# Kernel optimization log

Measured on AMD Instinct MI355X. Metric: run time of the kernel, lower is better.

## Reference

```python
import jax, jax.numpy as jnp
import numpy as np

LAMBDA_S = 1.0   # options['lambda_s']
NITER = 100      # options['iter_ihs']

_HS_FILTER = jnp.array([[1/12, 1/6, 1/12],
                        [1/6,  0.0, 1/6 ],
                        [1/12, 1/6, 1/12]], dtype=jnp.float32)


def _smooth(f):
    # f: [n, h, w] -> 3x3 Horn-Schunck weighted average, zero padding (== torch conv2d padding=1)
    k = _HS_FILTER.reshape(1, 1, 3, 3)  # [out_c, in_c, kh, kw]
    return jax.lax.conv_general_dilated(f[:, None], k, window_strides=(1, 1), padding='SAME')[:, 0]


def setup_inputs() -> dict:
    key = jax.random.key(0)
    k1, k2 = jax.random.split(key)
    n, h, w = 8, 256, 256
    x = jax.random.normal(k1, (n, 3, h, w), dtype=jnp.float32)            # [I_t, I_x, I_y]
    old_estimate = jax.random.normal(k2, (n, 2, h, w), dtype=jnp.float32)  # warm-start (u, v)
    return {"x": x, "old_estimate": old_estimate}


def reference(x, old_estimate):
    # x: [n,3,h,w]; old_estimate: [n,2,h,w]
    I_t, I_x, I_y = x[:, 0], x[:, 1], x[:, 2]
    denom = LAMBDA_S ** 2 + I_x ** 2 + I_y ** 2  # iteration-invariant
    u0, v0 = old_estimate[:, 0], old_estimate[:, 1]  # warm_ihs=True

    def step(carry, _):
        u, v = carry
        u_bar = _smooth(u)
        v_bar = _smooth(v)
        der = (I_x * u_bar + I_y * v_bar + I_t) / denom
        return (u_bar - I_x * der, v_bar - I_y * der), None

    (u, v), _ = jax.lax.scan(step, (u0, v0), None, length=NITER)
    return jnp.stack((u, v), axis=1)  # [n,2,h,w]
```

## Files before the change

### kernel.cpp

```cpp
#include <hip/hip_runtime.h>

typedef unsigned long long ull;

#define HH 256
#define WW 256
#define PLANE (HH*WW)
#define TILE_R 32
#define TILE_C 64
#define TT 8
#define ER (TILE_R + 2*TT)
#define EC (TILE_C + 2*TT)
#define NCP (EC/2)
#define NRG 12
#define RPT (ER/NRG)
#define NTHR 512
#define LSZ (4 + ER*EC*2 + 4)

#define RING_OFS (2u*1024u*1024u)
#define FLAG_OFS (4u*1024u*1024u)
#define RIMG (HH*(WW/2)*4)

__global__ __launch_bounds__(NTHR, 2)
void hs_mega(const float* __restrict__ x,
             const float* __restrict__ est,
             float* __restrict__ out,
             float* __restrict__ ws)
{
    __shared__ __align__(16) float s0[LSZ];
    __shared__ __align__(16) float s1[LSZ];

    const int img = blockIdx.x, cs = blockIdx.y, rb = blockIdx.z;
    const int tid = threadIdx.x;
    const int er0 = rb*TILE_R - TT;
    const int ec0 = cs*TILE_C - TT;
    const int blin = (img*4 + cs)*8 + rb;
    unsigned* flags = (unsigned*)(ws + FLAG_OFS);

    int nb = -1;
    if (tid < 8) {
        int t = (tid < 4) ? tid : tid + 1;
        int dr = t/3 - 1, dc = t%3 - 1;
        int nrb = rb + dr, ncs = cs + dc;
        if (nrb >= 0 && nrb < 8 && ncs >= 0 && ncs < 4)
            nb = (img*4 + ncs)*8 + nrb;
    }

    const int cp = tid % NCP;
    const int rg = tid / NCP;
    const bool active = (rg < NRG);
    const int r0   = (active ? rg : 0) * RPT;
    const int fb   = 4 + 4*cp;

    float2 ca[RPT], cb[RPT], cc[RPT], cd[RPT], ce[RPT];
    {
        const float* __restrict__ xit = x + img*3*PLANE;
        const float* __restrict__ xix = xit + PLANE;
        const float* __restrict__ xiy = xix + PLANE;
        #pragma unroll
        for (int i = 0; i < RPT; ++i) {
            int gr = er0 + r0 + i;
            #pragma unroll
            for (int j = 0; j < 2; ++j) {
                int gc = ec0 + 2*cp + j;
                float A=0.f, B=0.f, C=0.f, D=0.f, E=0.f;
                if (active && gr >= 0 && gr < HH && gc >= 0 && gc < WW) {
                    int q = gr*WW + gc;
                    float it = xit[q], ix = xix[q], iy = xiy[q];
                    float rd = 1.0f / (1.0f + ix*ix + iy*iy);
                    const float s12 = 1.0f/12.0f;
                    A = (1.0f - ix*ix*rd) * s12;
                    B = (ix*iy*rd) * s12;
                    C = ix*it*rd;
                    D = (1.0f - iy*iy*rd) * s12;
                    E = iy*it*rd;
                }
                if (j == 0) { ca[i].x=A; cb[i].x=B; cc[i].x=C; cd[i].x=D; ce[i].x=E; }
                else        { ca[i].y=A; cb[i].y=B; cc[i].y=C; cd[i].y=D; ce[i].y=E; }
            }
        }
    }

    {
        const float* __restrict__ eu = est + img*2*PLANE;
        const float* __restrict__ ev = eu + PLANE;
        for (int k = tid; k < ER*NCP; k += NTHR) {
            int r = k / NCP, c = k - r*NCP;
            int gr = er0 + r, gc = ec0 + 2*c;
            float2 uu = make_float2(0.f,0.f), vv = make_float2(0.f,0.f);
            if (gr >= 0 && gr < HH && gc >= 0 && gc < WW) {
                uu = *(const float2*)(eu + gr*WW + gc);
                vv = *(const float2*)(ev + gr*WW + gc);
            }
            *(float4*)(s0 + 4 + 160*r + 4*c) = make_float4(uu.x, vv.x, uu.y, vv.y);
        }
    }
    __syncthreads();

    for (int p = 0; p < 13; ++p) {
        const int niter = (p < 12) ? TT : 4;

        for (int s = 1; s <= niter; ++s) {
            const float* __restrict__ rbuf = ((s-1)&1) ? s1 : s0;
            float* __restrict__ wbuf = (s&1) ? s1 : s0;
            if (active) {
                const float* qb = rbuf + fb;

                const float* pr[RPT+2];
                {
                    int rm = (r0 == 0) ? 0 : r0 - 1;
                    pr[0] = qb + 160*rm;
                    pr[1] = qb + 160*r0;
                    #pragma unroll
                    for (int i = 0; i < RPT; ++i) {
                        int rr = r0 + i + 1;
                        if (rr > ER-1) rr = ER-1;
                        pr[i+2] = qb + 160*rr;
                    }
                }
                float2 L[RPT+2]; float4 M[RPT+2]; float2 R[RPT+2];
                #pragma unroll
                for (int i = 0; i < RPT+2; ++i) {
                    L[i] = *(const float2*)(pr[i] - 2);
                    M[i] = *(const float4*)(pr[i]);
                    R[i] = *(const float2*)(pr[i] + 4);
                }

                float2 hu[RPT+2], hv[RPT+2];
                #pragma unroll
                for (int i = 0; i < RPT+2; ++i) {
                    hu[i] = make_float2(fmaf(2.f, M[i].x, L[i].x) + M[i].z,
                                        fmaf(2.f, M[i].z, M[i].x) + R[i].x);
                    hv[i] = make_float2(fmaf(2.f, M[i].y, L[i].y) + M[i].w,
                                        fmaf(2.f, M[i].w, M[i].y) + R[i].y);
                }

                #pragma unroll
                for (int i = 0; i < RPT; ++i) {
                    float tux = fmaf(-4.f, M[i+1].x, fmaf(2.f, hu[i+1].x, hu[i].x) + hu[i+2].x);
                    float tuy = fmaf(-4.f, M[i+1].z, fmaf(2.f, hu[i+1].y, hu[i].y) + hu[i+2].y);
                    float tvx = fmaf(-4.f, M[i+1].y, fmaf(2.f, hv[i+1].x, hv[i].x) + hv[i+2].x);
                    float tvy = fmaf(-4.f, M[i+1].w, fmaf(2.f, hv[i+1].y, hv[i].y) + hv[i+2].y);
                    float2 un, vn;
                    un.x = fmaf(ca[i].x, tux, -fmaf(cb[i].x, tvx, cc[i].x));
                    un.y = fmaf(ca[i].y, tuy, -fmaf(cb[i].y, tvy, cc[i].y));
                    vn.x = fmaf(cd[i].x, tvx, -fmaf(cb[i].x, tux, ce[i].x));
                    vn.y = fmaf(cd[i].y, tvy, -fmaf(cb[i].y, tuy, ce[i].y));
                    *(float4*)(wbuf + 160*(r0 + i) + fb) = make_float4(un.x, vn.x, un.y, vn.y);
                }
            }
            __syncthreads();
        }

        if (p < 12) {
            float* ring = ws + (unsigned)(p & 1) * RING_OFS + img*RIMG;

            for (int k = tid; k < 640; k += NTHR) {
                int m = k; int r, c2;
                if (m < 256)      { r = m >> 5;              c2 = m & 31; }
                else if (m < 512) { r = 24 + ((m-256) >> 5); c2 = (m-256) & 31; }
                else { int mm = m - 512; r = 8 + (mm >> 3); int t = mm & 7; c2 = (t < 4) ? t : 24 + t; }
                const float* sp = s0 + 4 + 160*(r + TT) + 4*(c2 + 4);
                float* gp = ring + ((rb*TILE_R + r)*(WW/2) + cs*(TILE_C/2) + c2)*4;
                __hip_atomic_store((ull*)gp,     *(const ull*)sp,       __ATOMIC_RELAXED, __HIP_MEMORY_SCOPE_AGENT);
                __hip_atomic_store((ull*)gp + 1, *(const ull*)(sp + 2), __ATOMIC_RELAXED, __HIP_MEMORY_SCOPE_AGENT);
            }
            asm volatile("s_waitcnt vmcnt(0)" ::: "memory");
            __syncthreads();
            if (tid == 0)
                __hip_atomic_store(&flags[p*256 + blin], 0x5eed0100u + (unsigned)p,
                                   __ATOMIC_RELAXED, __HIP_MEMORY_SCOPE_AGENT);
            asm volatile("" ::: "memory");
            if (tid < 8 && nb >= 0) {
                const unsigned tgt = 0x5eed0100u + (unsigned)p;
                while (__hip_atomic_load(&flags[p*256 + nb],
                                         __ATOMIC_RELAXED, __HIP_MEMORY_SCOPE_AGENT) != tgt)
                    __builtin_amdgcn_s_sleep(1);
            }
            __syncthreads();

            for (int k = tid; k < 896; k += NTHR) {
                int m = k; int r, c2;
                if (m < 320)      { r = m / 40;              c2 = m - (m/40)*40; }
                else if (m < 640) { int mm = m-320; r = 40 + mm/40; c2 = mm - (mm/40)*40; }
                else { int mm = m - 640; r = 8 + (mm >> 3); int t = mm & 7; c2 = (t < 4) ? t : 32 + t; }
                int gr = er0 + r, gc2 = cs*(TILE_C/2) - 4 + c2;
                ull v0 = 0, v1 = 0;
                if (gr >= 0 && gr < HH && gc2 >= 0 && gc2 < WW/2) {
                    const float* gp = ring + (gr*(WW/2) + gc2)*4;
                    v0 = __hip_atomic_load((const ull*)gp,     __ATOMIC_RELAXED, __HIP_MEMORY_SCOPE_AGENT);
                    v1 = __hip_atomic_load((const ull*)gp + 1, __ATOMIC_RELAXED, __HIP_MEMORY_SCOPE_AGENT);
                }
                float* sp = s0 + 4 + 160*r + 4*c2;
                *(ull*)sp = v0;
                *(ull*)(sp + 2) = v1;
            }
            __syncthreads();
        }
    }

    {
        float* ou = out + img*2*PLANE;
        float* ov = ou + PLANE;
        for (int k = tid; k < 1024; k += NTHR) {
            int r = k >> 5, c2 = k & 31;
            float4 V = *(const float4*)(s0 + 4 + 160*(r + TT) + 4*(c2 + 4));
            int q = (rb*TILE_R + r)*WW + cs*TILE_C + 2*c2;
            *(float2*)(ou + q) = make_float2(V.x, V.z);
            *(float2*)(ov + q) = make_float2(V.y, V.w);
        }
    }
}

extern "C" void kernel_launch(void* const* d_in, const int* in_sizes, int n_in,
                              void* d_out, int out_size, void* d_ws, size_t ws_size,
                              hipStream_t stream) {
    const float* x   = (const float*)d_in[0];
    const float* est = (const float*)d_in[1];
    float* out = (float*)d_out;
    float* ws  = (float*)d_ws;

    dim3 grid(8, WW/TILE_C, HH/TILE_R);
    dim3 blk(NTHR);
    hs_mega<<<grid, blk, 0, stream>>>(x, est, out, ws);
}
```

Measured before the change: 196.9 us.

## Shrink halo compute region per sub-step and keep center rows in registers

Each temporal sub-step now computes only the rows and columns still valid within the shrinking trapezoid of the halo tile, and skips threads whose region is fully outside it. The centre values each thread owns are kept in registers (Mreg) across sub-steps instead of being re-read from LDS, so only boundary rows and left/right neighbours are loaded. This cuts redundant halo arithmetic and LDS reads. In exchange it adds per-row predication and divergence, and it assumes Mreg stays consistent for rows that were skipped in earlier steps.

```diff
diff --git a/kernel.cpp b/kernel.cpp
--- a/kernel.cpp
+++ b/kernel.cpp
@@ -96,56 +96,86 @@
     }
     __syncthreads();
 
+    float4 Mreg[RPT];
+
     for (int p = 0; p < 13; ++p) {
         const int niter = (p < 12) ? TT : 4;
+        const int m0 = TT - niter;
 
         for (int s = 1; s <= niter; ++s) {
             const float* __restrict__ rbuf = ((s-1)&1) ? s1 : s0;
             float* __restrict__ wbuf = (s&1) ? s1 : s0;
-            if (active) {
+            const int b = s + m0;
+            const int lo  = (r0 > b) ? r0 : b;
+            const int hi0 = r0 + RPT - 1;
+            const int hiB = ER - 1 - b;
+            const int hi  = (hi0 < hiB) ? hi0 : hiB;
+            const bool colOK = (2*cp + 1 >= b) && (2*cp <= EC - 1 - b);
+
+            if (active && colOK && lo <= hi) {
                 const float* qb = rbuf + fb;
 
-                const float* pr[RPT+2];
-                {
-                    int rm = (r0 == 0) ? 0 : r0 - 1;
-                    pr[0] = qb + 160*rm;
-                    pr[1] = qb + 160*r0;
-                    #pragma unroll
-                    for (int i = 0; i < RPT; ++i) {
-                        int rr = r0 + i + 1;
-                        if (rr > ER-1) rr = ER-1;
-                        pr[i+2] = qb + 160*rr;
-                    }
-                }
-                float2 L[RPT+2]; float4 M[RPT+2]; float2 R[RPT+2];
+                float2 L[RPT+2], R[RPT+2];
                 #pragma unroll
                 for (int i = 0; i < RPT+2; ++i) {
-                    L[i] = *(const float2*)(pr[i] - 2);
-                    M[i] = *(const float4*)(pr[i]);
-                    R[i] = *(const float2*)(pr[i] + 4);
+                    int row = r0 - 1 + i;
+                    if (row >= lo-1 && row <= hi+1) {
+                        const float* pr = qb + 160*row;
+                        L[i] = *(const float2*)(pr - 2);
+                        R[i] = *(const float2*)(pr + 4);
+                    }
+                }
+                float4 Mb0, MbN;
+                const bool needB0 = (r0 >= b);
+                const bool needBN = (hi0 <= hiB);
+                if (needB0) Mb0 = *(const float4*)(qb + 160*(r0-1));
+                if (needBN) MbN = *(const float4*)(qb + 160*(r0+RPT));
+                if (s == 1) {
+                    #pragma unroll
+                    for (int j = 0; j < RPT; ++j) {
+                        int row = r0 + j;
+                        if (row >= lo-1 && row <= hi+1)
+                            Mreg[j] = *(const float4*)(qb + 160*row);
+                    }
                 }
 
                 float2 hu[RPT+2], hv[RPT+2];
+                if (needB0) {
+                    hu[0] = make_float2(fmaf(2.f,Mb0.x,L[0].x)+Mb0.z, fmaf(2.f,Mb0.z,Mb0.x)+R[0].x);
+                    hv[0] = make_float2(fmaf(2.f,Mb0.y,L[0].y)+Mb0.w, fmaf(2.f,Mb0.w,Mb0.y)+R[0].y);
+                }
                 #pragma unroll
-                for (int i = 0; i < RPT+2; ++i) {
-                    hu[i] = make_float2(fmaf(2.f, M[i].x, L[i].x) + M[i].z,
-                                        fmaf(2.f, M[i].z, M[i].x) + R[i].x);
-                    hv[i] = make_float2(fmaf(2.f, M[i].y, L[i].y) + M[i].w,
-                                        fmaf(2.f, M[i].w, M[i].y) + R[i].y);
+                for (int j = 0; j < RPT; ++j) {
+                    int row = r0 + j;
+                    if (row >= lo-1 && row <= hi+1) {
+                        float4 Mc = Mreg[j];
+                        hu[j+1] = make_float2(fmaf(2.f,Mc.x,L[j+1].x)+Mc.z, fmaf(2.f,Mc.z,Mc.x)+R[j+1].x);
+                        hv[j+1] = make_float2(fmaf(2.f,Mc.y,L[j+1].y)+Mc.w, fmaf(2.f,Mc.w,Mc.y)+R[j+1].y);
+                    }
+                }
+                if (needBN) {
+                    hu[RPT+1] = make_float2(fmaf(2.f,MbN.x,L[RPT+1].x)+MbN.z, fmaf(2.f,MbN.z,MbN.x)+R[RPT+1].x);
+                    hv[RPT+1] = make_float2(fmaf(2.f,MbN.y,L[RPT+1].y)+MbN.w, fmaf(2.f,MbN.w,MbN.y)+R[RPT+1].y);
                 }
 
                 #pragma unroll
-                for (int i = 0; i < RPT; ++i) {
-                    float tux = fmaf(-4.f, M[i+1].x, fmaf(2.f, hu[i+1].x, hu[i].x) + hu[i+2].x);
-                    float tuy = fmaf(-4.f, M[i+1].z, fmaf(2.f, hu[i+1].y, hu[i].y) + hu[i+2].y);
-                    float tvx = fmaf(-4.f, M[i+1].y, fmaf(2.f, hv[i+1].x, hv[i].x) + hv[i+2].x);
-                    float tvy = fmaf(-4.f, M[i+1].w, fmaf(2.f, hv[i+1].y, hv[i].y) + hv[i+2].y);
-                    float2 un, vn;
-                    un.x = fmaf(ca[i].x, tux, -fmaf(cb[i].x, tvx, cc[i].x));
-                    un.y = fmaf(ca[i].y, tuy, -fmaf(cb[i].y, tvy, cc[i].y));
-                    vn.x = fmaf(cd[i].x, tvx, -fmaf(cb[i].x, tux, ce[i].x));
-                    vn.y = fmaf(cd[i].y, tvy, -fmaf(cb[i].y, tuy, ce[i].y));
-                    *(float4*)(wbuf + 160*(r0 + i) + fb) = make_float4(un.x, vn.x, un.y, vn.y);
+                for (int j = 0; j < RPT; ++j) {
+                    int row = r0 + j;
+                    if (row >= lo && row <= hi) {
+                        float4 Mc = Mreg[j];
+                        float tux = fmaf(-4.f, Mc.x, fmaf(2.f, hu[j+1].x, hu[j].x) + hu[j+2].x);
+                        float tuy = fmaf(-4.f, Mc.z, fmaf(2.f, hu[j+1].y, hu[j].y) + hu[j+2].y);
+                        float tvx = fmaf(-4.f, Mc.y, fmaf(2.f, hv[j+1].x, hv[j].x) + hv[j+2].x);
+                        float tvy = fmaf(-4.f, Mc.w, fmaf(2.f, hv[j+1].y, hv[j].y) + hv[j+2].y);
+                        float2 un, vn;
+                        un.x = fmaf(ca[j].x, tux, -fmaf(cb[j].x, tvx, cc[j].x));
+                        un.y = fmaf(ca[j].y, tuy, -fmaf(cb[j].y, tvy, cc[j].y));
+                        vn.x = fmaf(cd[j].x, tvx, -fmaf(cb[j].x, tux, ce[j].x));
+                        vn.y = fmaf(cd[j].y, tvy, -fmaf(cb[j].y, tuy, ce[j].y));
+                        float4 nv = make_float4(un.x, vn.x, un.y, vn.y);
+                        *(float4*)(wbuf + 160*row + fb) = nv;
+                        Mreg[j] = nv;
+                    }
                 }
             }
             __syncthreads();
```

Measured after the change: 224.7 us. 14.1% more time.
